# Kernel optimization log

Hardware: AMD Instinct MI355X
Metric: run time of the kernel (lower is better)

The kernel has to match this reference:

```python
import jax, jax.numpy as jnp
import numpy as np

N = 20000      # nodes
E = 640000     # edges (before self loops)
IN = 256       # in_channels == out_channels (forced by classifier size 4*in)
H1, C1 = 8, 16   # conv1: heads=8, out=16 -> concat 128
H2, C2 = 1, 256  # conv2: heads=1, out=out_channels
B = 4096       # article pairs
NEG_SLOPE = 0.2  # PyG GATv2Conv default negative_slope


def setup_inputs() -> dict:
    key = jax.random.key(0)
    ks = jax.random.split(key, 24)
    s = 0.05
    inp = {
        "gnn_x": jax.random.normal(ks[0], (N, IN), jnp.float32),
        "vanilla_x": jax.random.normal(ks[1], (N, IN), jnp.float32),
        "edge_src": jax.random.randint(ks[2], (E,), 0, N, jnp.int32),
        "edge_dst": jax.random.randint(ks[3], (E,), 0, N, jnp.int32),
        "a1_idx": jax.random.randint(ks[4], (B,), 0, N, jnp.int64),
        "a2_idx": jax.random.randint(ks[5], (B,), 0, N, jnp.int64),
        # conv1 params (lin_l, lin_r, att, bias)
        "Wl1": jax.random.normal(ks[6], (IN, H1 * C1), jnp.float32) * s,
        "bl1": jnp.zeros((H1 * C1,), jnp.float32),
        "Wr1": jax.random.normal(ks[7], (IN, H1 * C1), jnp.float32) * s,
        "br1": jnp.zeros((H1 * C1,), jnp.float32),
        "att1": jax.random.normal(ks[8], (H1, C1), jnp.float32) * s,
        "bias1": jnp.zeros((H1 * C1,), jnp.float32),
        # conv2 params
        "Wl2": jax.random.normal(ks[9], (H1 * C1, H2 * C2), jnp.float32) * s,
        "bl2": jnp.zeros((H2 * C2,), jnp.float32),
        "Wr2": jax.random.normal(ks[10], (H1 * C1, H2 * C2), jnp.float32) * s,
        "br2": jnp.zeros((H2 * C2,), jnp.float32),
        "att2": jax.random.normal(ks[11], (H2, C2), jnp.float32) * s,
        "bias2": jnp.zeros((H2 * C2,), jnp.float32),
        # classifier
        "Wc": jax.random.normal(ks[12], (4 * IN, 1), jnp.float32) * s,
        "bc": jnp.zeros((1,), jnp.float32),
    }
    return inp


def _gatv2_layer(x, src, dst, Wl, bl, Wr, br, att, bias):
    """GATv2Conv: x_l = lin_l(x)[src], x_r = lin_r(x)[dst];
    e = att . leaky_relu(x_l + x_r); segment softmax over dst; scatter-add x_l*alpha."""
    n = x.shape[0]
    h, c = att.shape
    xl = (x @ Wl + bl).reshape(n, h, c)
    xr = (x @ Wr + br).reshape(n, h, c)
    # per-edge attention logits [E, H]
    e = jnp.einsum('ehc,hc->eh', jax.nn.leaky_relu(xl[src] + xr[dst], NEG_SLOPE), att)
    # segment softmax over destination nodes (self loops guarantee non-empty segments)
    emax = jax.ops.segment_max(e, dst, num_segments=n)
    ex = jnp.exp(e - emax[dst])
    denom = jax.ops.segment_sum(ex, dst, num_segments=n)
    alpha = ex / denom[dst]                      # [E, H]
    out = jax.ops.segment_sum(alpha[:, :, None] * xl[src], dst, num_segments=n)  # [N,H,C]
    return out.reshape(n, h * c) + bias          # concat=True (heads=1 identical)


def reference(gnn_x, vanilla_x, Wl1, bl1, Wr1, br1, att1, bias1,
              Wl2, bl2, Wr2, br2, att2, bias2, Wc, bc,
              edge_src, edge_dst, a1_idx, a2_idx):
    n = gnn_x.shape[0]
    loops = jnp.arange(n, dtype=edge_src.dtype)
    src = jnp.concatenate([edge_src, loops])     # PyG add_self_loops=True
    dst = jnp.concatenate([edge_dst, loops])
    x = _gatv2_layer(gnn_x, src, dst, Wl1, bl1, Wr1, br1, att1, bias1)
    x = jax.nn.relu(x)
    x = _gatv2_layer(x, src, dst, Wl2, bl2, Wr2, br2, att2, bias2)
    combined = jnp.concatenate(
        [vanilla_x[a1_idx], vanilla_x[a2_idx], x[a1_idx], x[a2_idx]], axis=1)  # [B, 4*IN]
    logits = combined @ Wc + bc                  # [B, 1]
    return logits
```

## Files before the change

kernel.cpp:

```cpp
#include <hip/hip_runtime.h>
#include <math.h>

#define N_NODES 20000
#define M_PAD   20032
#define E_EDGES 640000
#define ET (E_EDGES + N_NODES)
#define IN_CH 256
#define D1 128
#define D2 256
#define BPAIRS 4096
#define NEG 0.2f
#define LOG2E 1.4426950408889634f

#define NB_HIST   128
#define CHUNK     ((ET + NB_HIST - 1) / NB_HIST)
#define HALF_BINS 10000

#define MARK_BLOCKS  (2 * BPAIRS / 256)
#define WCONV_BLOCKS 512
#define XCONV_BLOCKS (M_PAD * IN_CH / 4 / 4 / 256)

#if __has_builtin(__builtin_amdgcn_exp2f)
#define EXP2F(x) __builtin_amdgcn_exp2f(x)
#else
#define EXP2F(x) exp2f(x)
#endif

typedef __bf16 bf16x8 __attribute__((ext_vector_type(8)));
typedef float  f32x4  __attribute__((ext_vector_type(4)));
typedef float  f32x2  __attribute__((ext_vector_type(2)));
typedef unsigned short u16x4 __attribute__((ext_vector_type(4)));

__device__ __forceinline__ unsigned short f2b(float f) {
    unsigned int u = __float_as_uint(f);
    unsigned int r = u + 0x7FFFu + ((u >> 16) & 1u);
    return (unsigned short)(r >> 16);
}
__device__ __forceinline__ f32x2 up2(unsigned int u) {
    f32x2 r;
    r.x = __uint_as_float(u << 16);
    r.y = __uint_as_float(u & 0xFFFF0000u);
    return r;
}
__device__ __forceinline__ f32x2 lrelu2(f32x2 s) {
    return __builtin_elementwise_max(s, s * NEG);
}
__device__ __forceinline__ float lrelu(float s) { return fmaxf(s, NEG * s); }

__device__ __forceinline__ void unpack8(uint4 u, float* v) {
    v[0] = __uint_as_float(u.x << 16); v[1] = __uint_as_float(u.x & 0xFFFF0000u);
    v[2] = __uint_as_float(u.y << 16); v[3] = __uint_as_float(u.y & 0xFFFF0000u);
    v[4] = __uint_as_float(u.z << 16); v[5] = __uint_as_float(u.z & 0xFFFF0000u);
    v[6] = __uint_as_float(u.w << 16); v[7] = __uint_as_float(u.w & 0xFFFF0000u);
}


__global__ __launch_bounds__(256) void prep_kernel(
        const float* __restrict__ gnn_x,
        const float* __restrict__ Wl1, const float* __restrict__ Wr1,
        const float* __restrict__ Wl2, const float* __restrict__ Wr2,
        const int* __restrict__ edge_dst,
        const int* __restrict__ a1_raw, const int* __restrict__ a2_raw,
        unsigned short* __restrict__ xb,
        unsigned short* __restrict__ wt1l, unsigned short* __restrict__ wt1r,
        unsigned short* __restrict__ wt2l, unsigned short* __restrict__ wt2r,
        int* __restrict__ cb,
        int* __restrict__ rank,
        int* __restrict__ mark) {
    __shared__ int lc[HALF_BINS];
    int bid = blockIdx.x;
    if (bid < NB_HIST) {
        int ebeg = bid * CHUNK;
        int eend = min(ebeg + CHUNK, ET);
#pragma unroll 1
        for (int half = 0; half < 2; half++) {
            int lo = half * HALF_BINS;
            for (int i = threadIdx.x; i < HALF_BINS; i += 256) lc[i] = 0;
            __syncthreads();
            for (int e = ebeg + threadIdx.x; e < eend; e += 256) {
                int dst = (e < E_EDGES) ? edge_dst[e] : (e - E_EDGES);
                int d = dst - lo;
                if (0 <= d && d < HALF_BINS) rank[e] = atomicAdd(&lc[d], 1);
            }
            __syncthreads();
            for (int i = threadIdx.x; i < HALF_BINS; i += 256)
                cb[(size_t)bid * N_NODES + lo + i] = lc[i];
            __syncthreads();
        }
    } else if (bid < NB_HIST + MARK_BLOCKS) {
        int idx = (bid - NB_HIST) * 256 + threadIdx.x;
        __shared__ int stride_s;
        if (threadIdx.x == 0) {
            bool i64 = true;
            for (int i = 1; i < 63; i += 2) i64 = i64 && (a1_raw[i] == 0);
            stride_s = i64 ? 2 : 1;
        }
        __syncthreads();
        int stride = stride_s;
        if (idx < BPAIRS) mark[a1_raw[(long)idx * stride]] = 1;
        else mark[a2_raw[(long)(idx - BPAIRS) * stride]] = 1;
    } else if (bid < NB_HIST + MARK_BLOCKS + WCONV_BLOCKS) {
        int idx = (bid - NB_HIST - MARK_BLOCKS) * 256 + threadIdx.x;
        int seg = idx >> 15;
        int r = idx & 32767;
        const float* W;
        unsigned short* Wt;
        int k, n, K;
        if (seg < 2) {
            W = seg ? Wr1 : Wl1; Wt = seg ? wt1r : wt1l;
            k = r >> 7; n = r & 127; K = IN_CH;
        } else {
            W = (seg & 1) ? Wr2 : Wl2; Wt = (seg & 1) ? wt2r : wt2l;
            k = r >> 8; n = r & 255; K = D1;
        }
        Wt[n * K + k] = f2b(W[r]);
    } else {
        int tid = (bid - NB_HIST - MARK_BLOCKS - WCONV_BLOCKS) * 256
                + threadIdx.x;
        const int NQ = M_PAD * IN_CH / 4;
        int q0 = tid * 4;
#pragma unroll
        for (int j = 0; j < 4; j++) {
            int qi = q0 + j;
            if (qi >= NQ) break;
            int e0 = qi * 4;
            int row = e0 >> 8;
            u16x4 o;
            if (row < N_NODES) {
                f32x4 v = __builtin_nontemporal_load((const f32x4*)(gnn_x + e0));
                o.x = f2b(v.x); o.y = f2b(v.y); o.z = f2b(v.z); o.w = f2b(v.w);
            } else {
                o.x = o.y = o.z = o.w = 0;
            }
            *(u16x4*)(xb + e0) = o;
        }
    }
}


__global__ __launch_bounds__(256) void repprefix_kernel(
        int* __restrict__ cb, int* __restrict__ count) {
    int dst = blockIdx.x * 256 + threadIdx.x;
    if (dst >= N_NODES) return;
    int run = 0;
#pragma unroll 4
    for (int r = 0; r < NB_HIST; r++) {
        size_t idx = (size_t)r * N_NODES + dst;
        int c = cb[idx];
        cb[idx] = run;
        run += c;
    }
    count[dst] = run;
}


__global__ __launch_bounds__(1024) void scan_kernel(const int* __restrict__ count,
                                                    int* __restrict__ offsets) {
    const int PER = 20;
    int t = threadIdx.x;
    int base = t * PER;
    int local[PER];
    int sum = 0;
#pragma unroll
    for (int i = 0; i < PER; i++) {
        int idx = base + i;
        int v = (idx < N_NODES) ? count[idx] : 0;
        local[i] = sum;
        sum += v;
    }
    int lane = t & 63, wave = t >> 6;
    int s = sum;
#pragma unroll
    for (int off = 1; off < 64; off <<= 1) {
        int x = __shfl_up(s, off);
        if (lane >= off) s += x;
    }
    __shared__ int wsum[16];
    __shared__ int wpre[16];
    if (lane == 63) wsum[wave] = s;
    __syncthreads();
    if (t == 0) {
        int acc = 0;
        for (int w = 0; w < 16; w++) { wpre[w] = acc; acc += wsum[w]; }
        offsets[N_NODES] = acc;
    }
    __syncthreads();
    int thread_excl = wpre[wave] + (s - sum);
#pragma unroll
    for (int i = 0; i < PER; i++) {
        int idx = base + i;
        if (idx < N_NODES) offsets[idx] = thread_excl + local[i];
    }
}

__global__ void scatter_kernel(const int* __restrict__ edge_src,
                               const int* __restrict__ edge_dst,
                               const int* __restrict__ rank,
                               const int* __restrict__ offsets,
                               const int* __restrict__ cb,
                               int* __restrict__ sorted_src) {
    int e = blockIdx.x * blockDim.x + threadIdx.x;
    if (e >= ET) return;
    int dst = (e < E_EDGES) ? edge_dst[e] : (e - E_EDGES);
    int src = (e < E_EDGES) ? edge_src[e] : (e - E_EDGES);
    int rep = e / CHUNK;
    sorted_src[offsets[dst] + cb[(size_t)rep * N_NODES + dst] + rank[e]] = src;
}


template <int K>
__global__ __launch_bounds__(256) void dual_gemm_mfma_kernel(
        const unsigned short* __restrict__ A,
        const unsigned short* __restrict__ Wtl,
        const unsigned short* __restrict__ Wtr,
        const float* __restrict__ bl, const float* __restrict__ br,
        unsigned short* __restrict__ Yl, unsigned short* __restrict__ Yr,
        int M, int NOUT) {
    const int NK = K / 32;
    int wave = threadIdx.x >> 6;
    int lane = threadIdx.x & 63;
    int row0 = blockIdx.x * 64;
    int col0 = (blockIdx.y * 4 + wave) * 16;
    int rsub = lane & 15;
    int koff = (lane >> 4) * 8;

    const unsigned short* ap  = A   + (size_t)(row0 + rsub) * K + koff;
    const unsigned short* bpl = Wtl + (size_t)(col0 + rsub) * K + koff;
    const unsigned short* bpr = Wtr + (size_t)(col0 + rsub) * K + koff;

    bf16x8 bfl[NK], bfr[NK];
#pragma unroll
    for (int kb = 0; kb < NK; kb++) {
        bfl[kb] = *(const bf16x8*)(bpl + kb * 32);
        bfr[kb] = *(const bf16x8*)(bpr + kb * 32);
    }

    f32x4 l0 = {0.f, 0.f, 0.f, 0.f};
    f32x4 l1 = l0, l2 = l0, l3 = l0, r0 = l0, r1 = l0, r2 = l0, r3 = l0;

#pragma unroll
    for (int kb = 0; kb < NK; kb++) {
        int off = kb * 32;
        bf16x8 a0 = *(const bf16x8*)(ap + off);
        bf16x8 a1 = *(const bf16x8*)(ap + 16 * K + off);
        bf16x8 a2 = *(const bf16x8*)(ap + 32 * K + off);
        bf16x8 a3 = *(const bf16x8*)(ap + 48 * K + off);
        l0 = __builtin_amdgcn_mfma_f32_16x16x32_bf16(a0, bfl[kb], l0, 0, 0, 0);
        r0 = __builtin_amdgcn_mfma_f32_16x16x32_bf16(a0, bfr[kb], r0, 0, 0, 0);
        l1 = __builtin_amdgcn_mfma_f32_16x16x32_bf16(a1, bfl[kb], l1, 0, 0, 0);
        r1 = __builtin_amdgcn_mfma_f32_16x16x32_bf16(a1, bfr[kb], r1, 0, 0, 0);
        l2 = __builtin_amdgcn_mfma_f32_16x16x32_bf16(a2, bfl[kb], l2, 0, 0, 0);
        r2 = __builtin_amdgcn_mfma_f32_16x16x32_bf16(a2, bfr[kb], r2, 0, 0, 0);
        l3 = __builtin_amdgcn_mfma_f32_16x16x32_bf16(a3, bfl[kb], l3, 0, 0, 0);
        r3 = __builtin_amdgcn_mfma_f32_16x16x32_bf16(a3, bfr[kb], r3, 0, 0, 0);
    }

    int colg = col0 + rsub;
    float bvl = bl[colg];
    float bvr = br[colg];
    int rbase = row0 + (lane >> 4) * 4;
#pragma unroll
    for (int t = 0; t < 4; t++) {
        f32x4 al = (t == 0) ? l0 : (t == 1) ? l1 : (t == 2) ? l2 : l3;
        f32x4 ar = (t == 0) ? r0 : (t == 1) ? r1 : (t == 2) ? r2 : r3;
#pragma unroll
        for (int r = 0; r < 4; r++) {
            int row = rbase + t * 16 + r;
            if (row < M) {
                Yl[(size_t)row * NOUT + colg] = f2b(al[r] + bvl);
                Yr[(size_t)row * NOUT + colg] = f2b(ar[r] + bvr);
            }
        }
    }
}


__global__ __launch_bounds__(256) void aggregate1_kernel(
        const unsigned short* __restrict__ xl1, const unsigned short* __restrict__ xr1,
        const float* __restrict__ att1, const float* __restrict__ bias1,
        const int* __restrict__ offsets, const int* __restrict__ sorted_src,
        unsigned short* __restrict__ x1) {
    int wave = threadIdx.x >> 6;
    int lane = threadIdx.x & 63;
    int q = lane >> 4;
    int ql = lane & 15;
    int dst = blockIdx.x * 4 + wave;
    if (dst >= M_PAD) return;
    int c0 = ql * 8;
    if (dst >= N_NODES) {
        if (q == 0) {
            uint4 z; z.x = z.y = z.z = z.w = 0;
            *(uint4*)(x1 + (size_t)dst * D1 + c0) = z;
        }
        return;
    }

    uint4 xu = *(const uint4*)(xr1 + (size_t)dst * D1 + c0);
    f32x2 xr[4] = {up2(xu.x), up2(xu.y), up2(xu.z), up2(xu.w)};
    float4 aa0 = *(const float4*)(att1 + c0);
    float4 aa1 = *(const float4*)(att1 + c0 + 4);
    f32x2 att[4];
    att[0].x = aa0.x * LOG2E; att[0].y = aa0.y * LOG2E;
    att[1].x = aa0.z * LOG2E; att[1].y = aa0.w * LOG2E;
    att[2].x = aa1.x * LOG2E; att[2].y = aa1.y * LOG2E;
    att[3].x = aa1.z * LOG2E; att[3].y = aa1.w * LOG2E;

    int beg = offsets[dst], end = offsets[dst + 1];
    const unsigned short* base = xl1 + c0;

    float l = 0.f;
    f32x2 acc[4] = {{0.f,0.f},{0.f,0.f},{0.f,0.f},{0.f,0.f}};

    int i = beg;
    int s0 = sorted_src[min(i + q, end - 1)];
    uint4 g0 = *(const uint4*)(base + (size_t)s0 * D1);
    while (true) {
        int inext = i + 4;
        bool more = inext < end;
        uint4 g1;
        if (more) {
            int s1 = sorted_src[min(inext + q, end - 1)];
            g1 = *(const uint4*)(base + (size_t)s1 * D1);
        }
        bool act = (i + q) < end;
        f32x2 v0 = up2(g0.x), v1 = up2(g0.y), v2 = up2(g0.z), v3 = up2(g0.w);
        f32x2 p2 = att[0] * lrelu2(v0 + xr[0]);
        p2 += att[1] * lrelu2(v1 + xr[1]);
        p2 += att[2] * lrelu2(v2 + xr[2]);
        p2 += att[3] * lrelu2(v3 + xr[3]);
        float p = p2.x + p2.y;
        p += __shfl_xor(p, 1);
        float w = act ? EXP2F(p) : 0.f;
        l += w;
        acc[0] += w * v0; acc[1] += w * v1; acc[2] += w * v2; acc[3] += w * v3;
        if (!more) break;
        i = inext; g0 = g1;
    }
    l += __shfl_xor(l, 16);
    l += __shfl_xor(l, 32);
#pragma unroll
    for (int j = 0; j < 4; j++) {
        f32x2 t;
        t.x = __shfl_xor(acc[j].x, 16); t.y = __shfl_xor(acc[j].y, 16);
        acc[j] += t;
        t.x = __shfl_xor(acc[j].x, 32); t.y = __shfl_xor(acc[j].y, 32);
        acc[j] += t;
    }
    if (q == 0) {
        float inv = 1.f / l;
        float4 bb0 = *(const float4*)(bias1 + c0);
        float4 bb1 = *(const float4*)(bias1 + c0 + 4);
        unsigned short o[8];
        o[0] = f2b(fmaxf(acc[0].x * inv + bb0.x, 0.f));
        o[1] = f2b(fmaxf(acc[0].y * inv + bb0.y, 0.f));
        o[2] = f2b(fmaxf(acc[1].x * inv + bb0.z, 0.f));
        o[3] = f2b(fmaxf(acc[1].y * inv + bb0.w, 0.f));
        o[4] = f2b(fmaxf(acc[2].x * inv + bb1.x, 0.f));
        o[5] = f2b(fmaxf(acc[2].y * inv + bb1.y, 0.f));
        o[6] = f2b(fmaxf(acc[3].x * inv + bb1.z, 0.f));
        o[7] = f2b(fmaxf(acc[3].y * inv + bb1.w, 0.f));
        uint4 ov;
        ov.x = (unsigned int)o[0] | ((unsigned int)o[1] << 16);
        ov.y = (unsigned int)o[2] | ((unsigned int)o[3] << 16);
        ov.z = (unsigned int)o[4] | ((unsigned int)o[5] << 16);
        ov.w = (unsigned int)o[6] | ((unsigned int)o[7] << 16);
        *(uint4*)(x1 + (size_t)dst * D1 + c0) = ov;
    }
}


__global__ __launch_bounds__(256) void aggregate2_kernel(
        const unsigned short* __restrict__ xl2, const unsigned short* __restrict__ xr2,
        const float* __restrict__ att2, const float* __restrict__ bias2,
        const int* __restrict__ offsets, const int* __restrict__ sorted_src,
        const int* __restrict__ mark,
        float* __restrict__ x2) {
    int wave = threadIdx.x >> 6;
    int lane = threadIdx.x & 63;
    int half = lane >> 5;
    int hl = lane & 31;
    int dst = blockIdx.x * 4 + wave;
    if (dst >= N_NODES) return;
    if (!mark[dst]) return;
    int c0 = hl * 8;

    float xr[8], att[8];
    unpack8(*(const uint4*)(xr2 + (size_t)dst * D2 + c0), xr);
#pragma unroll
    for (int j = 0; j < 8; j++) att[j] = att2[c0 + j] * LOG2E;
    int beg = offsets[dst], end = offsets[dst + 1];

    float l = 0.f;
    float acc[8];
#pragma unroll
    for (int j = 0; j < 8; j++) acc[j] = 0.f;

    int i = beg;
    for (; i + 4 <= end; i += 4) {
        int sA = sorted_src[i + half];
        int sB = sorted_src[i + 2 + half];
        float vA[8], vB[8];
        unpack8(*(const uint4*)(xl2 + (size_t)sA * D2 + c0), vA);
        unpack8(*(const uint4*)(xl2 + (size_t)sB * D2 + c0), vB);
        float pA = 0.f, pB = 0.f;
#pragma unroll
        for (int j = 0; j < 8; j++) pA = fmaf(att[j], lrelu(vA[j] + xr[j]), pA);
#pragma unroll
        for (int j = 0; j < 8; j++) pB = fmaf(att[j], lrelu(vB[j] + xr[j]), pB);
        pA += __shfl_xor(pA, 1);  pB += __shfl_xor(pB, 1);
        pA += __shfl_xor(pA, 2);  pB += __shfl_xor(pB, 2);
        pA += __shfl_xor(pA, 4);  pB += __shfl_xor(pB, 4);
        pA += __shfl_xor(pA, 8);  pB += __shfl_xor(pB, 8);
        pA += __shfl_xor(pA, 16); pB += __shfl_xor(pB, 16);
        float wA = EXP2F(pA), wB = EXP2F(pB);
        l += wA + wB;
#pragma unroll
        for (int j = 0; j < 8; j++) acc[j] += wA * vA[j] + wB * vB[j];
    }
    for (; i + 2 <= end; i += 2) {
        int sA = sorted_src[i + half];
        float vA[8];
        unpack8(*(const uint4*)(xl2 + (size_t)sA * D2 + c0), vA);
        float pA = 0.f;
#pragma unroll
        for (int j = 0; j < 8; j++) pA = fmaf(att[j], lrelu(vA[j] + xr[j]), pA);
        pA += __shfl_xor(pA, 1);
        pA += __shfl_xor(pA, 2);
        pA += __shfl_xor(pA, 4);
        pA += __shfl_xor(pA, 8);
        pA += __shfl_xor(pA, 16);
        float wA = EXP2F(pA);
        l += wA;
#pragma unroll
        for (int j = 0; j < 8; j++) acc[j] += wA * vA[j];
    }
    if (i < end && half == 0) {
        int sA = sorted_src[i];
        float vA[8];
        unpack8(*(const uint4*)(xl2 + (size_t)sA * D2 + c0), vA);
        float pA = 0.f;
#pragma unroll
        for (int j = 0; j < 8; j++) pA = fmaf(att[j], lrelu(vA[j] + xr[j]), pA);
        pA += __shfl_xor(pA, 1);
        pA += __shfl_xor(pA, 2);
        pA += __shfl_xor(pA, 4);
        pA += __shfl_xor(pA, 8);
        pA += __shfl_xor(pA, 16);
        float wA = EXP2F(pA);
        l += wA;
#pragma unroll
        for (int j = 0; j < 8; j++) acc[j] += wA * vA[j];
    }
    l += __shfl_xor(l, 32);
#pragma unroll
    for (int j = 0; j < 8; j++) acc[j] += __shfl_xor(acc[j], 32);
    if (half == 0) {
        float inv = 1.f / l;
        float4 o0, o1;
        o0.x = acc[0] * inv + bias2[c0 + 0];
        o0.y = acc[1] * inv + bias2[c0 + 1];
        o0.z = acc[2] * inv + bias2[c0 + 2];
        o0.w = acc[3] * inv + bias2[c0 + 3];
        o1.x = acc[4] * inv + bias2[c0 + 4];
        o1.y = acc[5] * inv + bias2[c0 + 5];
        o1.z = acc[6] * inv + bias2[c0 + 6];
        o1.w = acc[7] * inv + bias2[c0 + 7];
        *(float4*)(x2 + (size_t)dst * D2 + c0) = o0;
        *(float4*)(x2 + (size_t)dst * D2 + c0 + 4) = o1;
    }
}


__global__ __launch_bounds__(256) void classifier_kernel(
        const float* __restrict__ vanilla_x, const float* __restrict__ x2,
        const int* __restrict__ a1_raw, const int* __restrict__ a2_raw,
        const float* __restrict__ Wc, const float* __restrict__ bc,
        float* __restrict__ out) {
    int b = blockIdx.x;
    int t = threadIdx.x;

    __shared__ int stride_s;
    if (t == 0) {
        bool i64 = true;
        for (int i = 1; i < 63; i += 2) i64 = i64 && (a1_raw[i] == 0);
        stride_s = i64 ? 2 : 1;
    }
    __syncthreads();
    int stride = stride_s;
    int a1 = a1_raw[(long)b * stride];
    int a2 = a2_raw[(long)b * stride];

    float s = vanilla_x[a1 * IN_CH + t] * Wc[t]
            + vanilla_x[a2 * IN_CH + t] * Wc[IN_CH + t]
            + x2[a1 * D2 + t] * Wc[2 * IN_CH + t]
            + x2[a2 * D2 + t] * Wc[3 * IN_CH + t];
    s += __shfl_xor(s, 1);
    s += __shfl_xor(s, 2);
    s += __shfl_xor(s, 4);
    s += __shfl_xor(s, 8);
    s += __shfl_xor(s, 16);
    s += __shfl_xor(s, 32);
    __shared__ float part[4];
    if ((t & 63) == 0) part[t >> 6] = s;
    __syncthreads();
    if (t == 0) out[b] = part[0] + part[1] + part[2] + part[3] + bc[0];
}


extern "C" void kernel_launch(void* const* d_in, const int* in_sizes, int n_in,
                              void* d_out, int out_size, void* d_ws, size_t ws_size,
                              hipStream_t stream) {
    const float* gnn_x     = (const float*)d_in[0];
    const float* vanilla_x = (const float*)d_in[1];
    const int*   edge_src  = (const int*)d_in[2];
    const int*   edge_dst  = (const int*)d_in[3];
    const int*   a1_idx    = (const int*)d_in[4];
    const int*   a2_idx    = (const int*)d_in[5];
    const float* Wl1   = (const float*)d_in[6];
    const float* bl1   = (const float*)d_in[7];
    const float* Wr1   = (const float*)d_in[8];
    const float* br1   = (const float*)d_in[9];
    const float* att1  = (const float*)d_in[10];
    const float* bias1 = (const float*)d_in[11];
    const float* Wl2   = (const float*)d_in[12];
    const float* bl2   = (const float*)d_in[13];
    const float* Wr2   = (const float*)d_in[14];
    const float* br2   = (const float*)d_in[15];
    const float* att2  = (const float*)d_in[16];
    const float* bias2 = (const float*)d_in[17];
    const float* Wc    = (const float*)d_in[18];
    const float* bc    = (const float*)d_in[19];
    float* out = (float*)d_out;

    char* p = (char*)d_ws;
    unsigned short* xb   = (unsigned short*)p; p += (size_t)M_PAD * IN_CH * 2;
    unsigned short* x1b  = (unsigned short*)p; p += (size_t)M_PAD * D1 * 2;
    unsigned short* xl1b = (unsigned short*)p; p += (size_t)N_NODES * D1 * 2;
    unsigned short* xr1b = (unsigned short*)p; p += (size_t)N_NODES * D1 * 2;
    unsigned short* xl2b = (unsigned short*)p; p += (size_t)N_NODES * D2 * 2;
    unsigned short* xr2b = (unsigned short*)p; p += (size_t)N_NODES * D2 * 2;
    unsigned short* wt1l = (unsigned short*)p; p += (size_t)D1 * IN_CH * 2;
    unsigned short* wt1r = (unsigned short*)p; p += (size_t)D1 * IN_CH * 2;
    unsigned short* wt2l = (unsigned short*)p; p += (size_t)D2 * D1 * 2;
    unsigned short* wt2r = (unsigned short*)p; p += (size_t)D2 * D1 * 2;
    float* x2 = (float*)p; p += (size_t)N_NODES * D2 * 4;
    int* count      = (int*)p; p += (size_t)N_NODES * 4;
    int* mark       = (int*)p; p += (size_t)N_NODES * 4;
    int* offsets    = (int*)p; p += (size_t)(N_NODES + 4) * 4;
    int* rank       = (int*)p; p += (size_t)ET * 4;
    int* sorted_src = (int*)p; p += (size_t)ET * 4;
    int* cb = (int*)xl2b;

    hipMemsetAsync(mark, 0, (size_t)N_NODES * sizeof(int), stream);

    prep_kernel<<<NB_HIST + MARK_BLOCKS + WCONV_BLOCKS + XCONV_BLOCKS,
                  256, 0, stream>>>(
        gnn_x, Wl1, Wr1, Wl2, Wr2, edge_dst, a1_idx, a2_idx,
        xb, wt1l, wt1r, wt2l, wt2r, cb, rank, mark);
    repprefix_kernel<<<(N_NODES + 255) / 256, 256, 0, stream>>>(cb, count);
    scan_kernel<<<1, 1024, 0, stream>>>(count, offsets);
    scatter_kernel<<<(ET + 255) / 256, 256, 0, stream>>>(
        edge_src, edge_dst, rank, offsets, cb, sorted_src);

    dim3 g1(M_PAD / 64, D1 / 64);
    dual_gemm_mfma_kernel<IN_CH><<<g1, 256, 0, stream>>>(
        xb, wt1l, wt1r, bl1, br1, xl1b, xr1b, N_NODES, D1);
    aggregate1_kernel<<<M_PAD / 4, 256, 0, stream>>>(
        xl1b, xr1b, att1, bias1, offsets, sorted_src, x1b);

    dim3 g2(M_PAD / 64, D2 / 64);
    dual_gemm_mfma_kernel<D1><<<g2, 256, 0, stream>>>(
        x1b, wt2l, wt2r, bl2, br2, xl2b, xr2b, N_NODES, D2);
    aggregate2_kernel<<<(N_NODES + 3) / 4, 256, 0, stream>>>(
        xl2b, xr2b, att2, bias2, offsets, sorted_src, mark, x2);

    classifier_kernel<<<BPAIRS, 256, 0, stream>>>(
        vanilla_x, x2, a1_idx, a2_idx, Wc, bc, out);
}
```

Measured before the change: 283.1 us.

## Fuse layer-1 GEMM with edge scatter, widen layer-2 GEMM tiles, drop mark memset

New measurement: 272.4 us. 3.8% less time.

```diff
diff --git a/kernel.cpp b/kernel.cpp
--- a/kernel.cpp
+++ b/kernel.cpp
@@ -19,6 +19,11 @@
 #define MARK_BLOCKS  (2 * BPAIRS / 256)
 #define WCONV_BLOCKS 512
 #define XCONV_BLOCKS (M_PAD * IN_CH / 4 / 4 / 256)
+
+#define G1X (M_PAD / 64)
+#define G1Y (D1 / 64)
+#define G1_BLOCKS (G1X * G1Y)
+#define SCAT_BLOCKS ((ET + 255) / 256)
 
 #if __has_builtin(__builtin_amdgcn_exp2f)
 #define EXP2F(x) __builtin_amdgcn_exp2f(x)
@@ -193,34 +198,20 @@
     }
 }
 
-__global__ void scatter_kernel(const int* __restrict__ edge_src,
-                               const int* __restrict__ edge_dst,
-                               const int* __restrict__ rank,
-                               const int* __restrict__ offsets,
-                               const int* __restrict__ cb,
-                               int* __restrict__ sorted_src) {
-    int e = blockIdx.x * blockDim.x + threadIdx.x;
-    if (e >= ET) return;
-    int dst = (e < E_EDGES) ? edge_dst[e] : (e - E_EDGES);
-    int src = (e < E_EDGES) ? edge_src[e] : (e - E_EDGES);
-    int rep = e / CHUNK;
-    sorted_src[offsets[dst] + cb[(size_t)rep * N_NODES + dst] + rank[e]] = src;
-}
-
 
 template <int K>
-__global__ __launch_bounds__(256) void dual_gemm_mfma_kernel(
+__device__ __forceinline__ void dual_gemm_tile(
         const unsigned short* __restrict__ A,
         const unsigned short* __restrict__ Wtl,
         const unsigned short* __restrict__ Wtr,
         const float* __restrict__ bl, const float* __restrict__ br,
         unsigned short* __restrict__ Yl, unsigned short* __restrict__ Yr,
-        int M, int NOUT) {
+        int M, int NOUT, int bx, int by) {
     const int NK = K / 32;
     int wave = threadIdx.x >> 6;
     int lane = threadIdx.x & 63;
-    int row0 = blockIdx.x * 64;
-    int col0 = (blockIdx.y * 4 + wave) * 16;
+    int row0 = bx * 64;
+    int col0 = (by * 4 + wave) * 16;
     int rsub = lane & 15;
     int koff = (lane >> 4) * 8;
 
@@ -269,6 +260,110 @@
             if (row < M) {
                 Yl[(size_t)row * NOUT + colg] = f2b(al[r] + bvl);
                 Yr[(size_t)row * NOUT + colg] = f2b(ar[r] + bvr);
+            }
+        }
+    }
+}
+
+
+__global__ __launch_bounds__(256) void gemm1_scatter_kernel(
+        const unsigned short* __restrict__ A,
+        const unsigned short* __restrict__ Wtl,
+        const unsigned short* __restrict__ Wtr,
+        const float* __restrict__ bl, const float* __restrict__ br,
+        unsigned short* __restrict__ Yl, unsigned short* __restrict__ Yr,
+        const int* __restrict__ edge_src, const int* __restrict__ edge_dst,
+        const int* __restrict__ rank, const int* __restrict__ offsets,
+        const int* __restrict__ cb, int* __restrict__ sorted_src) {
+    int bid = blockIdx.x;
+    if (bid < G1_BLOCKS) {
+        dual_gemm_tile<IN_CH>(A, Wtl, Wtr, bl, br, Yl, Yr,
+                              N_NODES, D1, bid % G1X, bid / G1X);
+    } else {
+        int e = (bid - G1_BLOCKS) * 256 + threadIdx.x;
+        if (e >= ET) return;
+        int dst = (e < E_EDGES) ? edge_dst[e] : (e - E_EDGES);
+        int src = (e < E_EDGES) ? edge_src[e] : (e - E_EDGES);
+        int rep = e / CHUNK;
+        sorted_src[offsets[dst] + cb[(size_t)rep * N_NODES + dst] + rank[e]] = src;
+    }
+}
+
+
+template <int K>
+__global__ __launch_bounds__(256) void dual_gemm_w32_kernel(
+        const unsigned short* __restrict__ A,
+        const unsigned short* __restrict__ Wtl,
+        const unsigned short* __restrict__ Wtr,
+        const float* __restrict__ bl, const float* __restrict__ br,
+        unsigned short* __restrict__ Yl, unsigned short* __restrict__ Yr,
+        int M, int NOUT) {
+    const int NK = K / 32;
+    int wave = threadIdx.x >> 6;
+    int lane = threadIdx.x & 63;
+    int row0 = blockIdx.x * 64;
+    int col0 = blockIdx.y * 128 + wave * 32;
+    int rsub = lane & 15;
+    int koff = (lane >> 4) * 8;
+
+    const unsigned short* ap = A + (size_t)(row0 + rsub) * K + koff;
+
+    bf16x8 bfl[2][NK], bfr[2][NK];
+#pragma unroll
+    for (int c = 0; c < 2; c++) {
+        const unsigned short* bpl = Wtl + (size_t)(col0 + c * 16 + rsub) * K + koff;
+        const unsigned short* bpr = Wtr + (size_t)(col0 + c * 16 + rsub) * K + koff;
+#pragma unroll
+        for (int kb = 0; kb < NK; kb++) {
+            bfl[c][kb] = *(const bf16x8*)(bpl + kb * 32);
+            bfr[c][kb] = *(const bf16x8*)(bpr + kb * 32);
+        }
+    }
+
+    f32x4 accl[2][4], accr[2][4];
+#pragma unroll
+    for (int c = 0; c < 2; c++)
+#pragma unroll
+        for (int t = 0; t < 4; t++) {
+            accl[c][t] = (f32x4){0.f, 0.f, 0.f, 0.f};
+            accr[c][t] = (f32x4){0.f, 0.f, 0.f, 0.f};
+        }
+
+#pragma unroll
+    for (int kb = 0; kb < NK; kb++) {
+        int off = kb * 32;
+        bf16x8 a[4];
+        a[0] = *(const bf16x8*)(ap + off);
+        a[1] = *(const bf16x8*)(ap + 16 * K + off);
+        a[2] = *(const bf16x8*)(ap + 32 * K + off);
+        a[3] = *(const bf16x8*)(ap + 48 * K + off);
+#pragma unroll
+        for (int t = 0; t < 4; t++) {
+#pragma unroll
+            for (int c = 0; c < 2; c++) {
+                accl[c][t] = __builtin_amdgcn_mfma_f32_16x16x32_bf16(
+                    a[t], bfl[c][kb], accl[c][t], 0, 0, 0);
+                accr[c][t] = __builtin_amdgcn_mfma_f32_16x16x32_bf16(
+                    a[t], bfr[c][kb], accr[c][t], 0, 0, 0);
+            }
+        }
+    }
+
+    int rbase = row0 + (lane >> 4) * 4;
+#pragma unroll
+    for (int c = 0; c < 2; c++) {
+        int colg = col0 + c * 16 + rsub;
+        float bvl = bl[colg];
+        float bvr = br[colg];
+#pragma unroll
+        for (int t = 0; t < 4; t++) {
+#pragma unroll
+            for (int r = 0; r < 4; r++) {
+                int row = rbase + t * 16 + r;
+                if (row < M) {
+                    Yl[(size_t)row * NOUT + colg] = f2b(accl[c][t][r] + bvl);
+                    Yr[(size_t)row * NOUT + colg] = f2b(accr[c][t][r] + bvr);
+                }
             }
         }
     }
@@ -381,7 +476,7 @@
     int hl = lane & 31;
     int dst = blockIdx.x * 4 + wave;
     if (dst >= N_NODES) return;
-    if (!mark[dst]) return;
+    if (mark[dst] != 1) return;
     int c0 = hl * 8;
 
     float xr[8], att[8];
@@ -551,25 +646,22 @@
     int* sorted_src = (int*)p; p += (size_t)ET * 4;
     int* cb = (int*)xl2b;
 
-    hipMemsetAsync(mark, 0, (size_t)N_NODES * sizeof(int), stream);
-
     prep_kernel<<<NB_HIST + MARK_BLOCKS + WCONV_BLOCKS + XCONV_BLOCKS,
                   256, 0, stream>>>(
         gnn_x, Wl1, Wr1, Wl2, Wr2, edge_dst, a1_idx, a2_idx,
         xb, wt1l, wt1r, wt2l, wt2r, cb, rank, mark);
     repprefix_kernel<<<(N_NODES + 255) / 256, 256, 0, stream>>>(cb, count);
     scan_kernel<<<1, 1024, 0, stream>>>(count, offsets);
-    scatter_kernel<<<(ET + 255) / 256, 256, 0, stream>>>(
+
+    gemm1_scatter_kernel<<<G1_BLOCKS + SCAT_BLOCKS, 256, 0, stream>>>(
+        xb, wt1l, wt1r, bl1, br1, xl1b, xr1b,
         edge_src, edge_dst, rank, offsets, cb, sorted_src);
 
-    dim3 g1(M_PAD / 64, D1 / 64);
-    dual_gemm_mfma_kernel<IN_CH><<<g1, 256, 0, stream>>>(
-        xb, wt1l, wt1r, bl1, br1, xl1b, xr1b, N_NODES, D1);
     aggregate1_kernel<<<M_PAD / 4, 256, 0, stream>>>(
         xl1b, xr1b, att1, bias1, offsets, sorted_src, x1b);
 
-    dim3 g2(M_PAD / 64, D2 / 64);
-    dual_gemm_mfma_kernel<D1><<<g2, 256, 0, stream>>>(
+    dim3 g2(M_PAD / 64, D2 / 128);
+    dual_gemm_w32_kernel<D1><<<g2, 256, 0, stream>>>(
         x1b, wt2l, wt2r, bl2, br2, xl2b, xr2b, N_NODES, D2);
     aggregate2_kernel<<<(N_NODES + 3) / 4, 256, 0, stream>>>(
         xl2b, xr2b, att2, bias2, offsets, sorted_src, mark, x2);
```
